# Optimization experiments

Measured on AMD Instinct MI355X. Metric: run time of the kernel, lower is better.

Reference implementation:

```python
import jax, jax.numpy as jnp
import numpy as np

PATCH = 14
LEVELS = 6
DIM = 512
MULT = 4
ITERS = 12
TOKEN_ATTEND_SELF_VALUE = -0.0005


def _grouped_ff(x, w1, b1, w2, b2):
    # x: [b, n, g, d]; per-group 1x1 conv == per-level MLP
    h = jnp.einsum('bnld,lmd->bnlm', x, w1) + b1  # [b,n,g,d*mult]
    h = jax.nn.gelu(h, approximate=False)
    return jnp.einsum('bnlm,ldm->bnld', h, w2) + b2


def _consensus(levels):
    # levels: [b, n, l, d]
    d = levels.shape[-1]
    n = levels.shape[1]
    k = levels / jnp.maximum(jnp.linalg.norm(levels, axis=-1, keepdims=True), 1e-12)
    sim = jnp.einsum('bild,bjld->blij', levels, k) * (d ** -0.5)
    self_mask = jnp.eye(n, dtype=bool)[None, None]  # attend_self=False
    sim = jnp.where(self_mask, TOKEN_ATTEND_SELF_VALUE, sim)
    attn = jax.nn.softmax(sim, axis=-1)
    return jnp.einsum('blij,bjld->bild', attn, levels)


def setup_inputs() -> dict:
    key = jax.random.key(0)
    ks = jax.random.split(key, 12)
    b, c, hw = 16, 1, 224
    pd = PATCH * PATCH * c  # 196
    nps = hw // PATCH
    n = nps * nps  # 256
    s = 0.02
    return {
        'img': jax.random.normal(ks[0], (b, c, hw, hw), jnp.float32),
        'to_tokens_w': jax.random.normal(ks[1], (pd, DIM), jnp.float32) * s,
        'to_tokens_b': jnp.zeros((DIM,), jnp.float32),
        'pos_emb': jax.random.normal(ks[2], (n, DIM), jnp.float32) * s,
        'init_levels': jax.random.normal(ks[3], (LEVELS, DIM), jnp.float32),
        'bu_w1': jax.random.normal(ks[4], (LEVELS, DIM * MULT, DIM), jnp.float32) * s,
        'bu_b1': jnp.zeros((LEVELS, DIM * MULT), jnp.float32),
        'bu_w2': jax.random.normal(ks[5], (LEVELS, DIM, DIM * MULT), jnp.float32) * s,
        'bu_b2': jnp.zeros((LEVELS, DIM), jnp.float32),
        'td_w1': jax.random.normal(ks[6], (LEVELS - 1, DIM * MULT, DIM), jnp.float32) * s,
        'td_b1': jnp.zeros((LEVELS - 1, DIM * MULT), jnp.float32),
        'td_w2': jax.random.normal(ks[7], (LEVELS - 1, DIM, DIM * MULT), jnp.float32) * s,
        'td_b2': jnp.zeros((LEVELS - 1, DIM), jnp.float32),
    }


def reference(img, to_tokens_w, to_tokens_b, pos_emb, init_levels,
              bu_w1, bu_b1, bu_w2, bu_b2, td_w1, td_b1, td_w2, td_b2):
    b, c, H, W = img.shape
    hp, wp = H // PATCH, W // PATCH
    n = hp * wp
    # b c (hp p1) (wp p2) -> b (hp wp) (p1 p2 c)
    x = img.reshape(b, c, hp, PATCH, wp, PATCH)
    x = x.transpose(0, 2, 4, 3, 5, 1).reshape(b, n, PATCH * PATCH * c)
    tokens = x @ to_tokens_w + to_tokens_b          # [b, n, d]
    pos = pos_emb[None, :, None, :]                 # [1, n, 1, d]
    bottom = tokens[:, :, None, :]                  # [b, n, 1, d]
    levels0 = jnp.broadcast_to(init_levels[None, None], (b, n, LEVELS, DIM))
    contrib = jnp.array([4., 4., 4., 4., 4., 3.], jnp.float32)[None, None, :, None]

    def step(levels, _):
        lwi = jnp.concatenate((bottom, levels), axis=2)         # [b, n, L+1, d]
        bu = _grouped_ff(lwi[:, :, :-1], bu_w1, bu_b1, bu_w2, bu_b2)
        td = _grouped_ff(lwi[:, :, 2:] + pos, td_w1, td_b1, td_w2, td_b2)
        td = jnp.pad(td, ((0, 0), (0, 0), (0, 1), (0, 0)))      # zero pad top level
        cons = _consensus(levels)
        new_levels = (levels + bu + td + cons) / contrib
        return new_levels, None

    levels, _ = jax.lax.scan(step, levels0, None, length=ITERS)
    return levels
```

## Files before the change

kernel.cpp:

```cpp
#include <hip/hip_runtime.h>
#include <hip/hip_bf16.h>
#include <math.h>

typedef unsigned short ushort_t;

#define DEV __device__ __forceinline__

DEV float bf2f(ushort_t u) {
  return __uint_as_float(((unsigned int)u) << 16);
}
DEV ushort_t f2bf(float f) {
  unsigned int x = __float_as_uint(f);
  return (ushort_t)((x + 0x7FFFu + ((x >> 16) & 1u)) >> 16);
}

DEV float gelu_f(float x) {
  float z = fabsf(x) * 0.70710678118654752f;
  float t = __builtin_amdgcn_rcpf(1.0f + 0.3275911f * z);
  float p = t * (0.254829592f +
            t * (-0.284496736f +
            t * (1.421413741f +
            t * (-1.453152027f +
            t * 1.061405429f))));
  float e = 1.0f - p * __expf(-z * z);
  float s = (x >= 0.f) ? e : -e;
  return 0.5f * x * (1.0f + s);
}

using bf16x8 = __attribute__((ext_vector_type(8))) __bf16;
using f32x4  = __attribute__((ext_vector_type(4))) float;

DEV void gload16(const ushort_t* g, ushort_t* l) {
  __builtin_amdgcn_global_load_lds((const __attribute__((address_space(1))) void*)g,
                                   (__attribute__((address_space(3))) void*)l, 16, 0, 0);
}

#define MFMA_QUAD(QM, QN)                                                      \
  _Pragma("unroll") for (int m_ = 0; m_ < 4; ++m_)                             \
  _Pragma("unroll") for (int n_ = 0; n_ < 2; ++n_)                             \
  _Pragma("unroll") for (int kk_ = 0; kk_ < 2; ++kk_)                          \
    acc[QM][QN][m_][n_] = __builtin_amdgcn_mfma_f32_16x16x32_bf16(             \
        aF[m_][kk_], bF[QN][n_][kk_], acc[QM][QN][m_][n_], 0, 0, 0);

template <typename F>
DEV void gemm256(const ushort_t* A, int lda, const ushort_t* B, int ldb, int K, F&& epi) {
  __shared__ alignas(16) ushort_t As[2][256 * 64];
  __shared__ alignas(16) ushort_t Bs[2][256 * 64];
  const int tid = threadIdx.x;
  const int lane = tid & 63;
  const int w = tid >> 6;
  const int ur = w >> 2, uc = w & 3;
  const int nk = K >> 6;

  const int c0 = tid, c1 = 512 + tid;
  const int row0 = c0 >> 3, row1 = c1 >> 3;
  const int sw0 = ((c0 & 7) ^ (row0 & 7)) * 8;
  const int sw1 = ((c1 & 7) ^ (row1 & 7)) * 8;
  const ushort_t* Ab0 = A + (size_t)row0 * lda + sw0;
  const ushort_t* Ab1 = A + (size_t)row1 * lda + sw1;
  const ushort_t* Bb0 = B + (size_t)row0 * ldb + sw0;
  const ushort_t* Bb1 = B + (size_t)row1 * ldb + sw1;
  const int ld0 = (0 * 512 + w * 64) * 8;
  const int ld1 = (1 * 512 + w * 64) * 8;

  auto stageA = [&](int t, int hh, int b) {
    const ushort_t* g0 = Ab0 + (size_t)hh * 128 * lda + t * 64;
    const ushort_t* g1 = Ab1 + (size_t)hh * 128 * lda + t * 64;
    ushort_t* l = &As[b][hh * 8192];
    gload16(g0, l + ld0);
    gload16(g1, l + ld1);
  };
  auto stageB = [&](int t, int hh, int b) {
    const ushort_t* g0 = Bb0 + (size_t)hh * 128 * ldb + t * 64;
    const ushort_t* g1 = Bb1 + (size_t)hh * 128 * ldb + t * 64;
    ushort_t* l = &Bs[b][hh * 8192];
    gload16(g0, l + ld0);
    gload16(g1, l + ld1);
  };

  int aoff[4][2], boff[2][2];
#pragma unroll
  for (int m = 0; m < 4; ++m)
#pragma unroll
    for (int kk = 0; kk < 2; ++kk) {
      int row = ur * 64 + m * 16 + (lane & 15);
      int ks = kk * 4 + (lane >> 4);
      aoff[m][kk] = row * 64 + ((ks ^ (lane & 7)) * 8);
    }
#pragma unroll
  for (int n = 0; n < 2; ++n)
#pragma unroll
    for (int kk = 0; kk < 2; ++kk) {
      int row = uc * 32 + n * 16 + (lane & 15);
      int ks = kk * 4 + (lane >> 4);
      boff[n][kk] = row * 64 + ((ks ^ (lane & 7)) * 8);
    }

  f32x4 acc[2][2][4][2];
#pragma unroll
  for (int qm = 0; qm < 2; ++qm)
#pragma unroll
    for (int qn = 0; qn < 2; ++qn)
#pragma unroll
      for (int m = 0; m < 4; ++m)
#pragma unroll
        for (int n = 0; n < 2; ++n) acc[qm][qn][m][n] = (f32x4){0.f, 0.f, 0.f, 0.f};

  stageA(0, 0, 0);
  stageB(0, 0, 0);
  stageB(0, 1, 0);
  stageA(0, 1, 0);
  stageA(1, 0, 1);
  stageB(1, 0, 1);
  asm volatile("s_waitcnt vmcnt(8)" ::: "memory");
  __builtin_amdgcn_s_barrier();

  bf16x8 aF[4][2], bF[2][2][2];

  for (int t = 0; t < nk; ++t) {
    const int b = t & 1;
    const ushort_t* asb = &As[b][0];
    const ushort_t* bsb = &Bs[b][0];
    const int t1 = (t + 1 < nk) ? t + 1 : nk - 1;
    const int t2 = (t + 2 < nk) ? t + 2 : nk - 1;

#pragma unroll
    for (int m = 0; m < 4; ++m)
#pragma unroll
      for (int kk = 0; kk < 2; ++kk) aF[m][kk] = *(const bf16x8*)&asb[aoff[m][kk]];
#pragma unroll
    for (int n = 0; n < 2; ++n)
#pragma unroll
      for (int kk = 0; kk < 2; ++kk) bF[0][n][kk] = *(const bf16x8*)&bsb[boff[n][kk]];
    stageB(t1, 1, (t + 1) & 1);
    __builtin_amdgcn_s_barrier();
    asm volatile("s_waitcnt lgkmcnt(0)" ::: "memory");
    __builtin_amdgcn_s_setprio(1);
    MFMA_QUAD(0, 0)
    __builtin_amdgcn_s_setprio(0);
    asm volatile("s_waitcnt vmcnt(8)" ::: "memory");
    __builtin_amdgcn_s_barrier();

#pragma unroll
    for (int n = 0; n < 2; ++n)
#pragma unroll
      for (int kk = 0; kk < 2; ++kk) bF[1][n][kk] = *(const bf16x8*)&bsb[boff[n][kk] + 8192];
    stageA(t1, 1, (t + 1) & 1);
    __builtin_amdgcn_s_barrier();
    asm volatile("s_waitcnt lgkmcnt(0)" ::: "memory");
    __builtin_amdgcn_s_setprio(1);
    MFMA_QUAD(0, 1)
    __builtin_amdgcn_s_setprio(0);
    asm volatile("s_waitcnt vmcnt(8)" ::: "memory");
    __builtin_amdgcn_s_barrier();

#pragma unroll
    for (int m = 0; m < 4; ++m)
#pragma unroll
      for (int kk = 0; kk < 2; ++kk) aF[m][kk] = *(const bf16x8*)&asb[aoff[m][kk] + 8192];
    stageA(t2, 0, b);
    __builtin_amdgcn_s_barrier();
    asm volatile("s_waitcnt lgkmcnt(0)" ::: "memory");
    __builtin_amdgcn_s_setprio(1);
    MFMA_QUAD(1, 0)
    __builtin_amdgcn_s_setprio(0);
    __builtin_amdgcn_s_barrier();

    stageB(t2, 0, b);
    __builtin_amdgcn_s_barrier();
    __builtin_amdgcn_s_setprio(1);
    MFMA_QUAD(1, 1)
    __builtin_amdgcn_s_setprio(0);
    asm volatile("s_waitcnt vmcnt(8)" ::: "memory");
    __builtin_amdgcn_s_barrier();
  }
  asm volatile("s_waitcnt vmcnt(0)" ::: "memory");

#pragma unroll
  for (int qm = 0; qm < 2; ++qm)
#pragma unroll
    for (int qn = 0; qn < 2; ++qn)
#pragma unroll
      for (int m = 0; m < 4; ++m)
#pragma unroll
        for (int n = 0; n < 2; ++n)
#pragma unroll
          for (int r = 0; r < 4; ++r) {
            int lr = qm * 128 + ur * 64 + m * 16 + (lane >> 4) * 4 + r;
            int lc = qn * 128 + uc * 32 + n * 16 + (lane & 15);
            epi(lr, lc, acc[qm][qn][m][n][r]);
          }
}

DEV void stage_tile(const ushort_t* g, int ld, ushort_t* lds, int t) {
  int w = t >> 6;
#pragma unroll
  for (int r = 0; r < 4; ++r) {
    int chunk = r * 256 + t;
    const ushort_t* gp = g + (size_t)(chunk >> 3) * ld + (size_t)(chunk & 7) * 8;
    ushort_t* lp = lds + (size_t)(r * 256 + w * 64) * 8;
    gload16(gp, lp);
  }
}

template <typename F>
DEV void gemm_tile(const ushort_t* A, int lda, const ushort_t* B, int ldb, int K, F&& epi) {
  __shared__ alignas(16) ushort_t As[128 * 64];
  __shared__ alignas(16) ushort_t Bs[128 * 64];
  int t = threadIdx.x;
  int lane = t & 63;
  int w = t >> 6;
  int wr = w >> 1, wc = w & 1;
  f32x4 zero = {0.f, 0.f, 0.f, 0.f};
  f32x4 acc[4][4];
#pragma unroll
  for (int m = 0; m < 4; ++m)
#pragma unroll
    for (int n = 0; n < 4; ++n) acc[m][n] = zero;

  for (int kt = 0; kt < K; kt += 64) {
    __syncthreads();
    stage_tile(A + kt, lda, As, t);
    stage_tile(B + kt, ldb, Bs, t);
    __syncthreads();
#pragma unroll
    for (int kk = 0; kk < 2; ++kk) {
      int kb = kk * 32 + (lane >> 4) * 8;
      bf16x8 af[4], bfr[4];
#pragma unroll
      for (int m = 0; m < 4; ++m)
        af[m] = *(const bf16x8*)&As[(size_t)(wr * 64 + m * 16 + (lane & 15)) * 64 + kb];
#pragma unroll
      for (int n = 0; n < 4; ++n)
        bfr[n] = *(const bf16x8*)&Bs[(size_t)(wc * 64 + n * 16 + (lane & 15)) * 64 + kb];
#pragma unroll
      for (int m = 0; m < 4; ++m)
#pragma unroll
        for (int n = 0; n < 4; ++n)
          acc[m][n] = __builtin_amdgcn_mfma_f32_16x16x32_bf16(af[m], bfr[n], acc[m][n], 0, 0, 0);
    }
  }
#pragma unroll
  for (int m = 0; m < 4; ++m)
#pragma unroll
    for (int n = 0; n < 4; ++n)
#pragma unroll
      for (int r = 0; r < 4; ++r) {
        int lr = wr * 64 + m * 16 + (lane >> 4) * 4 + r;
        int lc = wc * 64 + n * 16 + (lane & 15);
        epi(lr, lc, acc[m][n][r]);
      }
}

__global__ __launch_bounds__(256) void ff1_kernel(
    int g0, const ushort_t* tokens, const ushort_t* levels_bf, const ushort_t* levels_pos,
    const ushort_t* w1_bf, const float* bu_b1, const float* td_b1, ushort_t* h) {
  int g = g0 + blockIdx.z;
  int tm = blockIdx.x, tn = blockIdx.y;
  const ushort_t* A; int lda;
  if (g == 0)      { A = tokens     + (size_t)tm * 128 * 512;                              lda = 512;  }
  else if (g < 6)  { A = levels_bf  + (size_t)tm * 128 * 3072 + (size_t)(g - 1) * 512;     lda = 3072; }
  else             { A = levels_pos + (size_t)tm * 128 * 2560 + (size_t)(g - 6) * 512;     lda = 2560; }
  const ushort_t* W = w1_bf + (size_t)g * 2048 * 512 + (size_t)tn * 128 * 512;
  const float* bias = (g < 6) ? (bu_b1 + (size_t)g * 2048) : (td_b1 + (size_t)(g - 6) * 2048);
  ushort_t* out = h + ((size_t)(g - g0) * 4096 + (size_t)tm * 128) * 2048 + (size_t)tn * 128;
  gemm_tile(A, lda, W, 512, 512, [&](int lr, int lc, float v) {
    float x = v + bias[tn * 128 + lc];
    out[(size_t)lr * 2048 + lc] = f2bf(gelu_f(x));
  });
}

__global__ __launch_bounds__(512, 2) void ff2_kernel(
    int g0, const ushort_t* h, const ushort_t* w2_bf, const float* bu_b2, const float* td_b2,
    float* levels) {
  int g = g0 + blockIdx.z;
  int tm = blockIdx.x, tn = blockIdx.y;
  const ushort_t* A = h + ((size_t)(g - g0) * 4096 + (size_t)tm * 256) * 2048;
  const ushort_t* W = w2_bf + (size_t)g * 512 * 2048 + (size_t)tn * 256 * 2048;
  int l = (g < 6) ? g : (g - 6);
  const float* bias = (g < 6) ? (bu_b2 + (size_t)g * 512) : (td_b2 + (size_t)(g - 6) * 512);
  gemm256(A, 2048, W, 2048, 2048, [&](int lr, int lc, float v) {
    int bn = tm * 256 + lr;
    int d  = tn * 256 + lc;
    size_t idx = ((size_t)bn * 6 + l) * 512 + d;
    levels[idx] += v + bias[d];
  });
}

__global__ __launch_bounds__(256) void sim_kernel(const ushort_t* levels_bf, const float* invn,
                                                  ushort_t* simattn) {
  int bl = blockIdx.z; int tm = blockIdx.x, tn = blockIdx.y;
  int b = bl / 6, l = bl % 6;
  const ushort_t* A = levels_bf + ((size_t)(b * 256 + tm * 128) * 6 + l) * 512;
  const ushort_t* B = levels_bf + ((size_t)(b * 256 + tn * 128) * 6 + l) * 512;
  const float* inv = invn + (size_t)bl * 256;
  ushort_t* out = simattn + ((size_t)bl * 256 + tm * 128) * 256 + (size_t)tn * 128;
  gemm_tile(A, 3072, B, 3072, 512, [&](int lr, int lc, float v) {
    int i = tm * 128 + lr, j = tn * 128 + lc;
    float s = (i == j) ? -0.0005f : v * inv[j] * 0.044194173824159216f;
    out[(size_t)lr * 256 + lc] = f2bf(s);
  });
}

__global__ __launch_bounds__(256) void pv_kernel(const ushort_t* attn, const ushort_t* levelsT,
                                                 float* levels) {
  int bl = blockIdx.z; int tm = blockIdx.x, tn = blockIdx.y;
  int b = bl / 6, l = bl % 6;
  const ushort_t* A = attn + (size_t)bl * 256 * 256 + (size_t)tm * 128 * 256;
  const ushort_t* B = levelsT + ((size_t)bl * 512 + (size_t)tn * 128) * 256;
  gemm_tile(A, 256, B, 256, 256, [&](int lr, int lc, float v) {
    int n = tm * 128 + lr;
    int d = tn * 128 + lc;
    size_t idx = (((size_t)b * 256 + n) * 6 + l) * 512 + d;
    levels[idx] += v;
  });
}

__global__ __launch_bounds__(256) void softmax_kernel(ushort_t* simattn) {
  int row = blockIdx.x, t = threadIdx.x;
  __shared__ float red[256];
  float x = bf2f(simattn[(size_t)row * 256 + t]);
  red[t] = x;
  __syncthreads();
  for (int s = 128; s > 0; s >>= 1) { if (t < s) red[t] = fmaxf(red[t], red[t + s]); __syncthreads(); }
  float mx = red[0];
  __syncthreads();
  float e = expf(x - mx);
  red[t] = e;
  __syncthreads();
  for (int s = 128; s > 0; s >>= 1) { if (t < s) red[t] += red[t + s]; __syncthreads(); }
  float den = red[0];
  simattn[(size_t)row * 256 + t] = f2bf(e / den);
}

__global__ __launch_bounds__(128) void prep_kernel(float* levels, const float* pos_emb,
                                                   ushort_t* levels_bf, ushort_t* levels_pos,
                                                   float* invn, int apply) {
  int bid = blockIdx.x;
  int l = bid % 6;
  int bn = bid / 6;
  int n = bn & 255, b = bn >> 8;
  int t = threadIdx.x;
  float4 lv = *(const float4*)&levels[(size_t)bid * 512 + t * 4];
  if (apply) {
    float rc = (l == 5) ? (1.0f / 3.0f) : 0.25f;
    lv.x *= rc; lv.y *= rc; lv.z *= rc; lv.w *= rc;
    *(float4*)&levels[(size_t)bid * 512 + t * 4] = lv;
  }
  float ss = lv.x * lv.x + lv.y * lv.y + lv.z * lv.z + lv.w * lv.w;
#pragma unroll
  for (int off = 32; off > 0; off >>= 1) ss += __shfl_down(ss, off);
  __shared__ float s2[2];
  if ((t & 63) == 0) s2[t >> 6] = ss;
  __syncthreads();
  if (t == 0) {
    float tot = s2[0] + s2[1];
    invn[(size_t)(b * 6 + l) * 256 + n] = 1.0f / fmaxf(sqrtf(tot), 1e-12f);
  }
  ushort4 o;
  o.x = f2bf(lv.x); o.y = f2bf(lv.y); o.z = f2bf(lv.z); o.w = f2bf(lv.w);
  *(ushort4*)&levels_bf[(size_t)bid * 512 + t * 4] = o;
  if (l >= 1) {
    float4 pu = *(const float4*)&pos_emb[(size_t)n * 512 + t * 4];
    ushort4 op;
    op.x = f2bf(lv.x + pu.x);
    op.y = f2bf(lv.y + pu.y);
    op.z = f2bf(lv.z + pu.z);
    op.w = f2bf(lv.w + pu.w);
    *(ushort4*)&levels_pos[((size_t)bn * 5 + (l - 1)) * 512 + t * 4] = op;
  }
}

__global__ __launch_bounds__(256) void transpose_kernel(const float* levels, ushort_t* levelsT) {
  int bl = blockIdx.z; int b = bl / 6, l = bl % 6;
  int n0 = blockIdx.y * 64, d0 = blockIdx.x * 64;
  __shared__ ushort_t tile[64][72];
  int t = threadIdx.x;
#pragma unroll
  for (int rr = 0; rr < 2; ++rr) {
    int c = t + rr * 256;
    int r = c >> 3, c8 = (c & 7) * 8;
    const float* src = &levels[(((size_t)(b * 256 + n0 + r)) * 6 + l) * 512 + d0 + c8];
    float4 v0 = *(const float4*)src;
    float4 v1 = *(const float4*)(src + 4);
    tile[r][c8 + 0] = f2bf(v0.x); tile[r][c8 + 1] = f2bf(v0.y);
    tile[r][c8 + 2] = f2bf(v0.z); tile[r][c8 + 3] = f2bf(v0.w);
    tile[r][c8 + 4] = f2bf(v1.x); tile[r][c8 + 5] = f2bf(v1.y);
    tile[r][c8 + 6] = f2bf(v1.z); tile[r][c8 + 7] = f2bf(v1.w);
  }
  __syncthreads();
#pragma unroll
  for (int rr = 0; rr < 2; ++rr) {
    int c = t + rr * 256;
    int dr = c >> 3, n8 = (c & 7) * 8;
    ushort4 o0, o1;
    o0.x = tile[n8 + 0][dr]; o0.y = tile[n8 + 1][dr]; o0.z = tile[n8 + 2][dr]; o0.w = tile[n8 + 3][dr];
    o1.x = tile[n8 + 4][dr]; o1.y = tile[n8 + 5][dr]; o1.z = tile[n8 + 6][dr]; o1.w = tile[n8 + 7][dr];
    ushort_t* dst = &levelsT[((size_t)bl * 512 + d0 + dr) * 256 + n0 + n8];
    *(ushort4*)dst = o0;
    *(ushort4*)(dst + 4) = o1;
  }
}

__global__ __launch_bounds__(256) void tokens_kernel(const float* img, const float* ttw,
                                                     const float* ttb, ushort_t* tokens) {
  int token = blockIdx.x;
  int b = token >> 8, n = token & 255;
  int ph = n >> 4, pw = n & 15;
  __shared__ float patch[196];
  int t = threadIdx.x;
  if (t < 196) {
    int r = t / 14, cc = t % 14;
    patch[t] = img[(size_t)b * 50176 + (size_t)(ph * 14 + r) * 224 + pw * 14 + cc];
  }
  __syncthreads();
  float a0 = ttb[t];
  float a1 = ttb[t + 256];
  for (int k = 0; k < 196; ++k) {
    float p = patch[k];
    a0 += p * ttw[(size_t)k * 512 + t];
    a1 += p * ttw[(size_t)k * 512 + t + 256];
  }
  tokens[(size_t)token * 512 + t]       = f2bf(a0);
  tokens[(size_t)token * 512 + t + 256] = f2bf(a1);
}

__global__ void init_kernel(const float* init_levels, float* levels) {
  size_t i4 = (size_t)blockIdx.x * 256 + threadIdx.x;
  size_t e0 = i4 * 4;
  int idx = (int)(e0 % 3072);
  *(float4*)&levels[e0] = *(const float4*)&init_levels[idx];
}

__global__ void scale_kernel(float* levels) {
  size_t i4 = (size_t)blockIdx.x * 256 + threadIdx.x;
  size_t e0 = i4 * 4;
  int l = (int)((e0 >> 9) % 6);
  float rc = (l == 5) ? (1.0f / 3.0f) : 0.25f;
  float4 a = *(const float4*)&levels[e0];
  float4 o = {a.x * rc, a.y * rc, a.z * rc, a.w * rc};
  *(float4*)&levels[e0] = o;
}

__global__ void cvt_kernel(const float* src, ushort_t* dst, int n4) {
  int i = blockIdx.x * 256 + threadIdx.x;
  if (i >= n4) return;
  float4 v = ((const float4*)src)[i];
  ushort4 o;
  o.x = f2bf(v.x); o.y = f2bf(v.y); o.z = f2bf(v.z); o.w = f2bf(v.w);
  ((ushort4*)dst)[i] = o;
}

extern "C" void kernel_launch(void* const* d_in, const int* in_sizes, int n_in,
                              void* d_out, int out_size, void* d_ws, size_t ws_size,
                              hipStream_t stream) {
  const float* img    = (const float*)d_in[0];
  const float* ttw    = (const float*)d_in[1];
  const float* ttb    = (const float*)d_in[2];
  const float* pos    = (const float*)d_in[3];
  const float* initlv = (const float*)d_in[4];
  const float* bu_w1  = (const float*)d_in[5];
  const float* bu_b1  = (const float*)d_in[6];
  const float* bu_w2  = (const float*)d_in[7];
  const float* bu_b2  = (const float*)d_in[8];
  const float* td_w1  = (const float*)d_in[9];
  const float* td_b1  = (const float*)d_in[10];
  const float* td_w2  = (const float*)d_in[11];
  const float* td_b2  = (const float*)d_in[12];

  float* levels = (float*)d_out;

  char* p = (char*)d_ws;
  auto alloc = [&](size_t bytes) { char* r = p; p += (bytes + 255) & ~(size_t)255; return r; };
  float*    invn       = (float*)alloc(24576ull * 4);
  ushort_t* tokens     = (ushort_t*)alloc(2097152ull * 2);
  ushort_t* levels_bf  = (ushort_t*)alloc(12582912ull * 2);
  ushort_t* levels_pos = (ushort_t*)alloc(10485760ull * 2);
  ushort_t* levelsT    = (ushort_t*)alloc(12582912ull * 2);
  ushort_t* simattn    = (ushort_t*)alloc(6291456ull * 2);
  ushort_t* w1_bf      = (ushort_t*)alloc(11534336ull * 2);
  ushort_t* w2_bf      = (ushort_t*)alloc(11534336ull * 2);
  size_t used = (size_t)(p - (char*)d_ws);
  if (used + 16777216ull > ws_size) return;
  size_t hbytes = ws_size - used;
  int gpp = (int)(hbytes / 16777216ull);
  if (gpp > 6) gpp = 6;
  ushort_t* h = (ushort_t*)alloc((size_t)gpp * 16777216ull);

  cvt_kernel<<<6144, 256, 0, stream>>>(bu_w1, w1_bf, 1572864);
  cvt_kernel<<<5120, 256, 0, stream>>>(td_w1, w1_bf + 6291456ull, 1310720);
  cvt_kernel<<<6144, 256, 0, stream>>>(bu_w2, w2_bf, 1572864);
  cvt_kernel<<<5120, 256, 0, stream>>>(td_w2, w2_bf + 6291456ull, 1310720);
  tokens_kernel<<<4096, 256, 0, stream>>>(img, ttw, ttb, tokens);
  init_kernel<<<12288, 256, 0, stream>>>(initlv, levels);

  for (int it = 0; it < 12; ++it) {
    prep_kernel<<<24576, 128, 0, stream>>>(levels, pos, levels_bf, levels_pos, invn,
                                           it > 0 ? 1 : 0);
    transpose_kernel<<<dim3(8, 4, 96), 256, 0, stream>>>(levels, levelsT);
    sim_kernel<<<dim3(2, 2, 96), 256, 0, stream>>>(levels_bf, invn, simattn);
    softmax_kernel<<<24576, 256, 0, stream>>>(simattn);
    pv_kernel<<<dim3(2, 4, 96), 256, 0, stream>>>(simattn, levelsT, levels);
    for (int g0 = 0; g0 < 11; g0 += gpp) {
      int gn = 11 - g0 < gpp ? 11 - g0 : gpp;
      ff1_kernel<<<dim3(32, 16, gn), 256, 0, stream>>>(g0, tokens, levels_bf, levels_pos,
                                                       w1_bf, bu_b1, td_b1, h);
      ff2_kernel<<<dim3(16, 2, gn), 512, 0, stream>>>(g0, h, w2_bf, bu_b2, td_b2, levels);
    }
  }
  scale_kernel<<<12288, 256, 0, stream>>>(levels);
}
```

Measured before the change: 5.540 ms.

## Fuse similarity and softmax, enlarge FF1 tiles, batch all FF groups

Replaces the separate sim GEMM and row-softmax kernels with one kernel that computes a full 128x256 similarity tile per block and does the row max/sum reduction in registers and shared memory. This removes a round trip of the bf16 score matrix through global memory and one launch per iteration. FF1 moves to a 256x256 tile GEMM with 512 threads but drops double buffering, so loads are no longer overlapped with compute. When the workspace is large enough, all 11 groups are launched at once rather than in chunks of six, giving fewer and larger launches. The fused kernel exposes fewer blocks, which may lower occupancy.

```diff
diff --git a/kernel.cpp b/kernel.cpp
--- a/kernel.cpp
+++ b/kernel.cpp
@@ -33,6 +33,76 @@
 DEV void gload16(const ushort_t* g, ushort_t* l) {
   __builtin_amdgcn_global_load_lds((const __attribute__((address_space(1))) void*)g,
                                    (__attribute__((address_space(3))) void*)l, 16, 0, 0);
+}
+
+DEV void stage256(const ushort_t* g, int ld, ushort_t* lds, int t) {
+  int w = t >> 6;
+#pragma unroll
+  for (int r = 0; r < 4; ++r) {
+    int chunk = r * 512 + t;
+    const ushort_t* gp = g + (size_t)(chunk >> 3) * ld + (size_t)(chunk & 7) * 8;
+    ushort_t* lp = lds + (size_t)(r * 512 + w * 64) * 8;
+    gload16(gp, lp);
+  }
+}
+
+DEV void stage128_512(const ushort_t* g, int ld, ushort_t* lds, int t) {
+  int w = t >> 6;
+#pragma unroll
+  for (int r = 0; r < 2; ++r) {
+    int chunk = r * 512 + t;
+    const ushort_t* gp = g + (size_t)(chunk >> 3) * ld + (size_t)(chunk & 7) * 8;
+    ushort_t* lp = lds + (size_t)(r * 512 + w * 64) * 8;
+    gload16(gp, lp);
+  }
+}
+
+template <typename F>
+DEV void gemm256_2ph(const ushort_t* A, int lda, const ushort_t* B, int ldb, int K, F&& epi) {
+  __shared__ alignas(16) ushort_t As[256 * 64];
+  __shared__ alignas(16) ushort_t Bs[256 * 64];
+  int t = threadIdx.x;
+  int lane = t & 63;
+  int w = t >> 6;
+  int ur = w >> 2, uc = w & 3;
+  f32x4 acc[8][4];
+#pragma unroll
+  for (int m = 0; m < 8; ++m)
+#pragma unroll
+    for (int n = 0; n < 4; ++n) acc[m][n] = (f32x4){0.f, 0.f, 0.f, 0.f};
+
+  for (int kt = 0; kt < K; kt += 64) {
+    __syncthreads();
+    stage256(A + kt, lda, As, t);
+    stage256(B + kt, ldb, Bs, t);
+    __syncthreads();
+#pragma unroll
+    for (int kk = 0; kk < 2; ++kk) {
+      int kb = kk * 32 + (lane >> 4) * 8;
+      bf16x8 af[8], bfr[4];
+#pragma unroll
+      for (int m = 0; m < 8; ++m)
+        af[m] = *(const bf16x8*)&As[(size_t)(ur * 128 + m * 16 + (lane & 15)) * 64 + kb];
+#pragma unroll
+      for (int n = 0; n < 4; ++n)
+        bfr[n] = *(const bf16x8*)&Bs[(size_t)(uc * 64 + n * 16 + (lane & 15)) * 64 + kb];
+#pragma unroll
+      for (int m = 0; m < 8; ++m)
+#pragma unroll
+        for (int n = 0; n < 4; ++n)
+          acc[m][n] = __builtin_amdgcn_mfma_f32_16x16x32_bf16(af[m], bfr[n], acc[m][n], 0, 0, 0);
+    }
+  }
+#pragma unroll
+  for (int m = 0; m < 8; ++m)
+#pragma unroll
+    for (int n = 0; n < 4; ++n)
+#pragma unroll
+      for (int r = 0; r < 4; ++r) {
+        int lr = ur * 128 + m * 16 + (lane >> 4) * 4 + r;
+        int lc = uc * 64 + n * 16 + (lane & 15);
+        epi(lr, lc, acc[m][n][r]);
+      }
 }
 
 #define MFMA_QUAD(QM, QN)                                                      \
@@ -252,20 +322,20 @@
       }
 }
 
-__global__ __launch_bounds__(256) void ff1_kernel(
+__global__ __launch_bounds__(512, 2) void ff1_kernel(
     int g0, const ushort_t* tokens, const ushort_t* levels_bf, const ushort_t* levels_pos,
     const ushort_t* w1_bf, const float* bu_b1, const float* td_b1, ushort_t* h) {
   int g = g0 + blockIdx.z;
   int tm = blockIdx.x, tn = blockIdx.y;
   const ushort_t* A; int lda;
-  if (g == 0)      { A = tokens     + (size_t)tm * 128 * 512;                              lda = 512;  }
-  else if (g < 6)  { A = levels_bf  + (size_t)tm * 128 * 3072 + (size_t)(g - 1) * 512;     lda = 3072; }
-  else             { A = levels_pos + (size_t)tm * 128 * 2560 + (size_t)(g - 6) * 512;     lda = 2560; }
-  const ushort_t* W = w1_bf + (size_t)g * 2048 * 512 + (size_t)tn * 128 * 512;
+  if (g == 0)      { A = tokens     + (size_t)tm * 256 * 512;                              lda = 512;  }
+  else if (g < 6)  { A = levels_bf  + (size_t)tm * 256 * 3072 + (size_t)(g - 1) * 512;     lda = 3072; }
+  else             { A = levels_pos + (size_t)tm * 256 * 2560 + (size_t)(g - 6) * 512;     lda = 2560; }
+  const ushort_t* W = w1_bf + (size_t)g * 2048 * 512 + (size_t)tn * 256 * 512;
   const float* bias = (g < 6) ? (bu_b1 + (size_t)g * 2048) : (td_b1 + (size_t)(g - 6) * 2048);
-  ushort_t* out = h + ((size_t)(g - g0) * 4096 + (size_t)tm * 128) * 2048 + (size_t)tn * 128;
-  gemm_tile(A, lda, W, 512, 512, [&](int lr, int lc, float v) {
-    float x = v + bias[tn * 128 + lc];
+  ushort_t* out = h + ((size_t)(g - g0) * 4096 + (size_t)tm * 256) * 2048 + (size_t)tn * 256;
+  gemm256_2ph(A, lda, W, 512, 512, [&](int lr, int lc, float v) {
+    float x = v + bias[tn * 256 + lc];
     out[(size_t)lr * 2048 + lc] = f2bf(gelu_f(x));
   });
 }
@@ -287,19 +357,143 @@
   });
 }
 
-__global__ __launch_bounds__(256) void sim_kernel(const ushort_t* levels_bf, const float* invn,
-                                                  ushort_t* simattn) {
-  int bl = blockIdx.z; int tm = blockIdx.x, tn = blockIdx.y;
+__global__ __launch_bounds__(512) void simsm_kernel(const ushort_t* levels_bf, const float* invn,
+                                                    ushort_t* attn) {
+  int tm = blockIdx.x;
+  int bl = blockIdx.y;
   int b = bl / 6, l = bl % 6;
   const ushort_t* A = levels_bf + ((size_t)(b * 256 + tm * 128) * 6 + l) * 512;
-  const ushort_t* B = levels_bf + ((size_t)(b * 256 + tn * 128) * 6 + l) * 512;
+  const ushort_t* B = levels_bf + ((size_t)(b * 256) * 6 + l) * 512;
   const float* inv = invn + (size_t)bl * 256;
-  ushort_t* out = simattn + ((size_t)bl * 256 + tm * 128) * 256 + (size_t)tn * 128;
-  gemm_tile(A, 3072, B, 3072, 512, [&](int lr, int lc, float v) {
-    int i = tm * 128 + lr, j = tn * 128 + lc;
-    float s = (i == j) ? -0.0005f : v * inv[j] * 0.044194173824159216f;
-    out[(size_t)lr * 256 + lc] = f2bf(s);
-  });
+  ushort_t* out = attn + ((size_t)(bl * 256 + tm * 128)) * 256;
+
+  __shared__ alignas(16) ushort_t As[128 * 64];
+  __shared__ alignas(16) ushort_t Bs[256 * 64];
+  __shared__ alignas(16) float red[128][4];
+
+  int t = threadIdx.x, lane = t & 63, w = t >> 6;
+  int ur = w >> 2, uc = w & 3;
+  f32x4 acc[4][4];
+#pragma unroll
+  for (int m = 0; m < 4; ++m)
+#pragma unroll
+    for (int n = 0; n < 4; ++n) acc[m][n] = (f32x4){0.f, 0.f, 0.f, 0.f};
+
+  for (int kt = 0; kt < 512; kt += 64) {
+    __syncthreads();
+    stage128_512(A + kt, 3072, As, t);
+    stage256(B + kt, 3072, Bs, t);
+    __syncthreads();
+#pragma unroll
+    for (int kk = 0; kk < 2; ++kk) {
+      int kb = kk * 32 + (lane >> 4) * 8;
+      bf16x8 af[4], bfr[4];
+#pragma unroll
+      for (int m = 0; m < 4; ++m)
+        af[m] = *(const bf16x8*)&As[(size_t)(ur * 64 + m * 16 + (lane & 15)) * 64 + kb];
+#pragma unroll
+      for (int n = 0; n < 4; ++n)
+        bfr[n] = *(const bf16x8*)&Bs[(size_t)(uc * 64 + n * 16 + (lane & 15)) * 64 + kb];
+#pragma unroll
+      for (int m = 0; m < 4; ++m)
+#pragma unroll
+        for (int n = 0; n < 4; ++n)
+          acc[m][n] = __builtin_amdgcn_mfma_f32_16x16x32_bf16(af[m], bfr[n], acc[m][n], 0, 0, 0);
+    }
+  }
+
+  float invv[4];
+#pragma unroll
+  for (int n = 0; n < 4; ++n)
+    invv[n] = inv[uc * 64 + n * 16 + (lane & 15)] * 0.044194173824159216f;
+  float rowm[4][4];
+#pragma unroll
+  for (int m = 0; m < 4; ++m)
+#pragma unroll
+    for (int r = 0; r < 4; ++r) rowm[m][r] = -3.0e38f;
+#pragma unroll
+  for (int m = 0; m < 4; ++m)
+#pragma unroll
+    for (int n = 0; n < 4; ++n)
+#pragma unroll
+      for (int r = 0; r < 4; ++r) {
+        int i = tm * 128 + ur * 64 + m * 16 + (lane >> 4) * 4 + r;
+        int j = uc * 64 + n * 16 + (lane & 15);
+        float v = (i == j) ? -0.0005f : acc[m][n][r] * invv[n];
+        acc[m][n][r] = v;
+        rowm[m][r] = fmaxf(rowm[m][r], v);
+      }
+#pragma unroll
+  for (int off = 1; off < 16; off <<= 1)
+#pragma unroll
+    for (int m = 0; m < 4; ++m)
+#pragma unroll
+      for (int r = 0; r < 4; ++r) rowm[m][r] = fmaxf(rowm[m][r], __shfl_xor(rowm[m][r], off));
+  if ((lane & 15) == 0) {
+#pragma unroll
+    for (int m = 0; m < 4; ++m)
+#pragma unroll
+      for (int r = 0; r < 4; ++r)
+        red[ur * 64 + m * 16 + (lane >> 4) * 4 + r][uc] = rowm[m][r];
+  }
+  __syncthreads();
+  float rmax[4][4];
+#pragma unroll
+  for (int m = 0; m < 4; ++m)
+#pragma unroll
+    for (int r = 0; r < 4; ++r) {
+      float4 p = *(const float4*)&red[ur * 64 + m * 16 + (lane >> 4) * 4 + r][0];
+      rmax[m][r] = fmaxf(fmaxf(p.x, p.y), fmaxf(p.z, p.w));
+    }
+  __syncthreads();
+
+  float rows[4][4];
+#pragma unroll
+  for (int m = 0; m < 4; ++m)
+#pragma unroll
+    for (int r = 0; r < 4; ++r) rows[m][r] = 0.f;
+#pragma unroll
+  for (int m = 0; m < 4; ++m)
+#pragma unroll
+    for (int n = 0; n < 4; ++n)
+#pragma unroll
+      for (int r = 0; r < 4; ++r) {
+        float e = __expf(acc[m][n][r] - rmax[m][r]);
+        acc[m][n][r] = e;
+        rows[m][r] += e;
+      }
+#pragma unroll
+  for (int off = 1; off < 16; off <<= 1)
+#pragma unroll
+    for (int m = 0; m < 4; ++m)
+#pragma unroll
+      for (int r = 0; r < 4; ++r) rows[m][r] += __shfl_xor(rows[m][r], off);
+  if ((lane & 15) == 0) {
+#pragma unroll
+    for (int m = 0; m < 4; ++m)
+#pragma unroll
+      for (int r = 0; r < 4; ++r)
+        red[ur * 64 + m * 16 + (lane >> 4) * 4 + r][uc] = rows[m][r];
+  }
+  __syncthreads();
+  float rden[4][4];
+#pragma unroll
+  for (int m = 0; m < 4; ++m)
+#pragma unroll
+    for (int r = 0; r < 4; ++r) {
+      float4 p = *(const float4*)&red[ur * 64 + m * 16 + (lane >> 4) * 4 + r][0];
+      rden[m][r] = __builtin_amdgcn_rcpf(p.x + p.y + p.z + p.w);
+    }
+#pragma unroll
+  for (int m = 0; m < 4; ++m)
+#pragma unroll
+    for (int n = 0; n < 4; ++n)
+#pragma unroll
+      for (int r = 0; r < 4; ++r) {
+        int lr = ur * 64 + m * 16 + (lane >> 4) * 4 + r;
+        int lc = uc * 64 + n * 16 + (lane & 15);
+        out[(size_t)lr * 256 + lc] = f2bf(acc[m][n][r] * rden[m][r]);
+      }
 }
 
 __global__ __launch_bounds__(256) void pv_kernel(const ushort_t* attn, const ushort_t* levelsT,
@@ -314,23 +508,6 @@
     size_t idx = (((size_t)b * 256 + n) * 6 + l) * 512 + d;
     levels[idx] += v;
   });
-}
-
-__global__ __launch_bounds__(256) void softmax_kernel(ushort_t* simattn) {
-  int row = blockIdx.x, t = threadIdx.x;
-  __shared__ float red[256];
-  float x = bf2f(simattn[(size_t)row * 256 + t]);
-  red[t] = x;
-  __syncthreads();
-  for (int s = 128; s > 0; s >>= 1) { if (t < s) red[t] = fmaxf(red[t], red[t + s]); __syncthreads(); }
-  float mx = red[0];
-  __syncthreads();
-  float e = expf(x - mx);
-  red[t] = e;
-  __syncthreads();
-  for (int s = 128; s > 0; s >>= 1) { if (t < s) red[t] += red[t + s]; __syncthreads(); }
-  float den = red[0];
-  simattn[(size_t)row * 256 + t] = f2bf(e / den);
 }
 
 __global__ __launch_bounds__(128) void prep_kernel(float* levels, const float* pos_emb,
@@ -483,9 +660,9 @@
   size_t used = (size_t)(p - (char*)d_ws);
   if (used + 16777216ull > ws_size) return;
   size_t hbytes = ws_size - used;
-  int gpp = (int)(hbytes / 16777216ull);
-  if (gpp > 6) gpp = 6;
-  ushort_t* h = (ushort_t*)alloc((size_t)gpp * 16777216ull);
+  int hgroups = (int)(hbytes / 16777216ull);
+  if (hgroups > 11) hgroups = 11;
+  ushort_t* h = (ushort_t*)alloc((size_t)hgroups * 16777216ull);
 
   cvt_kernel<<<6144, 256, 0, stream>>>(bu_w1, w1_bf, 1572864);
   cvt_kernel<<<5120, 256, 0, stream>>>(td_w1, w1_bf + 6291456ull, 1310720);
@@ -498,14 +675,22 @@
     prep_kernel<<<24576, 128, 0, stream>>>(levels, pos, levels_bf, levels_pos, invn,
                                            it > 0 ? 1 : 0);
     transpose_kernel<<<dim3(8, 4, 96), 256, 0, stream>>>(levels, levelsT);
-    sim_kernel<<<dim3(2, 2, 96), 256, 0, stream>>>(levels_bf, invn, simattn);
-    softmax_kernel<<<24576, 256, 0, stream>>>(simattn);
+    simsm_kernel<<<dim3(2, 96), 512, 0, stream>>>(levels_bf, invn, simattn);
     pv_kernel<<<dim3(2, 4, 96), 256, 0, stream>>>(simattn, levelsT, levels);
-    for (int g0 = 0; g0 < 11; g0 += gpp) {
-      int gn = 11 - g0 < gpp ? 11 - g0 : gpp;
-      ff1_kernel<<<dim3(32, 16, gn), 256, 0, stream>>>(g0, tokens, levels_bf, levels_pos,
-                                                       w1_bf, bu_b1, td_b1, h);
-      ff2_kernel<<<dim3(16, 2, gn), 512, 0, stream>>>(g0, h, w2_bf, bu_b2, td_b2, levels);
+    if (hgroups >= 11) {
+      ff1_kernel<<<dim3(16, 8, 11), 512, 0, stream>>>(0, tokens, levels_bf, levels_pos,
+                                                      w1_bf, bu_b1, td_b1, h);
+      ff2_kernel<<<dim3(16, 2, 6), 512, 0, stream>>>(0, h, w2_bf, bu_b2, td_b2, levels);
+      ff2_kernel<<<dim3(16, 2, 5), 512, 0, stream>>>(6, h + 50331648ull, w2_bf,
+                                                     bu_b2, td_b2, levels);
+    } else {
+      int gpp = hgroups < 6 ? hgroups : 6;
+      for (int g0 = 0; g0 < 11; g0 += gpp) {
+        int gn = 11 - g0 < gpp ? 11 - g0 : gpp;
+        ff1_kernel<<<dim3(16, 8, gn), 512, 0, stream>>>(g0, tokens, levels_bf, levels_pos,
+                                                        w1_bf, bu_b1, td_b1, h);
+        ff2_kernel<<<dim3(16, 2, gn), 512, 0, stream>>>(g0, h, w2_bf, bu_b2, td_b2, levels);
+      }
     }
   }
   scale_kernel<<<12288, 256, 0, stream>>>(levels);
```

Measured after the change: 5.969 ms. +7.8%, slower.

## Use 256x256 single-buffer GEMM tiles for FF1 and batch all FF groups per launch

Applied to the files above, without the earlier changes.

FF1 moves from 128x128 tiles with 256 threads to a new 256x256 tile GEMM with 512 threads, which stages both operands into LDS and computes 8x4 MFMA fragments per wave. This raises data reuse per tile at the cost of no double buffering. The top-down FF2 outputs are now written to a separate fp32 buffer and added in prep/scale, which removes the read-modify-write race across levels. With that in place, all 11 groups can run in one launch when workspace allows. Softmax also switches to the fast __expf.

```diff
diff --git a/kernel.cpp b/kernel.cpp
--- a/kernel.cpp
+++ b/kernel.cpp
@@ -33,6 +33,65 @@
 DEV void gload16(const ushort_t* g, ushort_t* l) {
   __builtin_amdgcn_global_load_lds((const __attribute__((address_space(1))) void*)g,
                                    (__attribute__((address_space(3))) void*)l, 16, 0, 0);
+}
+
+DEV void stage256(const ushort_t* g, int ld, ushort_t* lds, int t) {
+  int w = t >> 6;
+#pragma unroll
+  for (int r = 0; r < 4; ++r) {
+    int chunk = r * 512 + t;
+    const ushort_t* gp = g + (size_t)(chunk >> 3) * ld + (size_t)(chunk & 7) * 8;
+    ushort_t* lp = lds + (size_t)(r * 512 + w * 64) * 8;
+    gload16(gp, lp);
+  }
+}
+
+template <typename F>
+DEV void gemm256_2ph(const ushort_t* A, int lda, const ushort_t* B, int ldb, int K, F&& epi) {
+  __shared__ alignas(16) ushort_t As[256 * 64];
+  __shared__ alignas(16) ushort_t Bs[256 * 64];
+  int t = threadIdx.x;
+  int lane = t & 63;
+  int w = t >> 6;
+  int ur = w >> 2, uc = w & 3;
+  f32x4 acc[8][4];
+#pragma unroll
+  for (int m = 0; m < 8; ++m)
+#pragma unroll
+    for (int n = 0; n < 4; ++n) acc[m][n] = (f32x4){0.f, 0.f, 0.f, 0.f};
+
+  for (int kt = 0; kt < K; kt += 64) {
+    __syncthreads();
+    stage256(A + kt, lda, As, t);
+    stage256(B + kt, ldb, Bs, t);
+    __syncthreads();
+#pragma unroll
+    for (int kk = 0; kk < 2; ++kk) {
+      int kb = kk * 32 + (lane >> 4) * 8;
+      bf16x8 af[8], bfr[4];
+#pragma unroll
+      for (int m = 0; m < 8; ++m)
+        af[m] = *(const bf16x8*)&As[(size_t)(ur * 128 + m * 16 + (lane & 15)) * 64 + kb];
+#pragma unroll
+      for (int n = 0; n < 4; ++n)
+        bfr[n] = *(const bf16x8*)&Bs[(size_t)(uc * 64 + n * 16 + (lane & 15)) * 64 + kb];
+#pragma unroll
+      for (int m = 0; m < 8; ++m)
+#pragma unroll
+        for (int n = 0; n < 4; ++n)
+          acc[m][n] = __builtin_amdgcn_mfma_f32_16x16x32_bf16(af[m], bfr[n], acc[m][n], 0, 0, 0);
+    }
+  }
+#pragma unroll
+  for (int m = 0; m < 8; ++m)
+#pragma unroll
+    for (int n = 0; n < 4; ++n)
+#pragma unroll
+      for (int r = 0; r < 4; ++r) {
+        int lr = ur * 128 + m * 16 + (lane >> 4) * 4 + r;
+        int lc = uc * 64 + n * 16 + (lane & 15);
+        epi(lr, lc, acc[m][n][r]);
+      }
 }
 
 #define MFMA_QUAD(QM, QN)                                                      \
@@ -252,38 +311,40 @@
       }
 }
 
-__global__ __launch_bounds__(256) void ff1_kernel(
+__global__ __launch_bounds__(512, 2) void ff1_kernel(
     int g0, const ushort_t* tokens, const ushort_t* levels_bf, const ushort_t* levels_pos,
     const ushort_t* w1_bf, const float* bu_b1, const float* td_b1, ushort_t* h) {
   int g = g0 + blockIdx.z;
   int tm = blockIdx.x, tn = blockIdx.y;
   const ushort_t* A; int lda;
-  if (g == 0)      { A = tokens     + (size_t)tm * 128 * 512;                              lda = 512;  }
-  else if (g < 6)  { A = levels_bf  + (size_t)tm * 128 * 3072 + (size_t)(g - 1) * 512;     lda = 3072; }
-  else             { A = levels_pos + (size_t)tm * 128 * 2560 + (size_t)(g - 6) * 512;     lda = 2560; }
-  const ushort_t* W = w1_bf + (size_t)g * 2048 * 512 + (size_t)tn * 128 * 512;
+  if (g == 0)      { A = tokens     + (size_t)tm * 256 * 512;                              lda = 512;  }
+  else if (g < 6)  { A = levels_bf  + (size_t)tm * 256 * 3072 + (size_t)(g - 1) * 512;     lda = 3072; }
+  else             { A = levels_pos + (size_t)tm * 256 * 2560 + (size_t)(g - 6) * 512;     lda = 2560; }
+  const ushort_t* W = w1_bf + (size_t)g * 2048 * 512 + (size_t)tn * 256 * 512;
   const float* bias = (g < 6) ? (bu_b1 + (size_t)g * 2048) : (td_b1 + (size_t)(g - 6) * 2048);
-  ushort_t* out = h + ((size_t)(g - g0) * 4096 + (size_t)tm * 128) * 2048 + (size_t)tn * 128;
-  gemm_tile(A, lda, W, 512, 512, [&](int lr, int lc, float v) {
-    float x = v + bias[tn * 128 + lc];
+  ushort_t* out = h + ((size_t)(g - g0) * 4096 + (size_t)tm * 256) * 2048 + (size_t)tn * 256;
+  gemm256_2ph(A, lda, W, 512, 512, [&](int lr, int lc, float v) {
+    float x = v + bias[tn * 256 + lc];
     out[(size_t)lr * 2048 + lc] = f2bf(gelu_f(x));
   });
 }
 
 __global__ __launch_bounds__(512, 2) void ff2_kernel(
     int g0, const ushort_t* h, const ushort_t* w2_bf, const float* bu_b2, const float* td_b2,
-    float* levels) {
+    float* levels, float* tdbuf) {
   int g = g0 + blockIdx.z;
   int tm = blockIdx.x, tn = blockIdx.y;
   const ushort_t* A = h + ((size_t)(g - g0) * 4096 + (size_t)tm * 256) * 2048;
   const ushort_t* W = w2_bf + (size_t)g * 512 * 2048 + (size_t)tn * 256 * 2048;
   int l = (g < 6) ? g : (g - 6);
   const float* bias = (g < 6) ? (bu_b2 + (size_t)g * 512) : (td_b2 + (size_t)(g - 6) * 512);
+  bool to_td = (g >= 6) && (tdbuf != nullptr);
   gemm256(A, 2048, W, 2048, 2048, [&](int lr, int lc, float v) {
     int bn = tm * 256 + lr;
     int d  = tn * 256 + lc;
-    size_t idx = ((size_t)bn * 6 + l) * 512 + d;
-    levels[idx] += v + bias[d];
+    float r = v + bias[d];
+    if (to_td) tdbuf[((size_t)bn * 5 + l) * 512 + d] = r;
+    else       levels[((size_t)bn * 6 + l) * 512 + d] += r;
   });
 }
 
@@ -302,6 +363,23 @@
   });
 }
 
+__global__ __launch_bounds__(256) void softmax_kernel(ushort_t* simattn) {
+  int row = blockIdx.x, t = threadIdx.x;
+  __shared__ float red[256];
+  float x = bf2f(simattn[(size_t)row * 256 + t]);
+  red[t] = x;
+  __syncthreads();
+  for (int s = 128; s > 0; s >>= 1) { if (t < s) red[t] = fmaxf(red[t], red[t + s]); __syncthreads(); }
+  float mx = red[0];
+  __syncthreads();
+  float e = __expf(x - mx);
+  red[t] = e;
+  __syncthreads();
+  for (int s = 128; s > 0; s >>= 1) { if (t < s) red[t] += red[t + s]; __syncthreads(); }
+  float den = red[0];
+  simattn[(size_t)row * 256 + t] = f2bf(e / den);
+}
+
 __global__ __launch_bounds__(256) void pv_kernel(const ushort_t* attn, const ushort_t* levelsT,
                                                  float* levels) {
   int bl = blockIdx.z; int tm = blockIdx.x, tn = blockIdx.y;
@@ -316,26 +394,9 @@
   });
 }
 
-__global__ __launch_bounds__(256) void softmax_kernel(ushort_t* simattn) {
-  int row = blockIdx.x, t = threadIdx.x;
-  __shared__ float red[256];
-  float x = bf2f(simattn[(size_t)row * 256 + t]);
-  red[t] = x;
-  __syncthreads();
-  for (int s = 128; s > 0; s >>= 1) { if (t < s) red[t] = fmaxf(red[t], red[t + s]); __syncthreads(); }
-  float mx = red[0];
-  __syncthreads();
-  float e = expf(x - mx);
-  red[t] = e;
-  __syncthreads();
-  for (int s = 128; s > 0; s >>= 1) { if (t < s) red[t] += red[t + s]; __syncthreads(); }
-  float den = red[0];
-  simattn[(size_t)row * 256 + t] = f2bf(e / den);
-}
-
 __global__ __launch_bounds__(128) void prep_kernel(float* levels, const float* pos_emb,
                                                    ushort_t* levels_bf, ushort_t* levels_pos,
-                                                   float* invn, int apply) {
+                                                   float* invn, const float* tdbuf, int apply) {
   int bid = blockIdx.x;
   int l = bid % 6;
   int bn = bid / 6;
@@ -343,6 +404,10 @@
   int t = threadIdx.x;
   float4 lv = *(const float4*)&levels[(size_t)bid * 512 + t * 4];
   if (apply) {
+    if (tdbuf != nullptr && l < 5) {
+      float4 td = *(const float4*)&tdbuf[((size_t)bn * 5 + l) * 512 + t * 4];
+      lv.x += td.x; lv.y += td.y; lv.z += td.z; lv.w += td.w;
+    }
     float rc = (l == 5) ? (1.0f / 3.0f) : 0.25f;
     lv.x *= rc; lv.y *= rc; lv.z *= rc; lv.w *= rc;
     *(float4*)&levels[(size_t)bid * 512 + t * 4] = lv;
@@ -432,12 +497,18 @@
   *(float4*)&levels[e0] = *(const float4*)&init_levels[idx];
 }
 
-__global__ void scale_kernel(float* levels) {
+__global__ void scale_kernel(float* levels, const float* tdbuf) {
   size_t i4 = (size_t)blockIdx.x * 256 + threadIdx.x;
   size_t e0 = i4 * 4;
   int l = (int)((e0 >> 9) % 6);
+  size_t bn = e0 / 3072;
+  int d = (int)(e0 & 511);
+  float4 a = *(const float4*)&levels[e0];
+  if (tdbuf != nullptr && l < 5) {
+    float4 td = *(const float4*)&tdbuf[((size_t)bn * 5 + l) * 512 + d];
+    a.x += td.x; a.y += td.y; a.z += td.z; a.w += td.w;
+  }
   float rc = (l == 5) ? (1.0f / 3.0f) : 0.25f;
-  float4 a = *(const float4*)&levels[e0];
   float4 o = {a.x * rc, a.y * rc, a.z * rc, a.w * rc};
   *(float4*)&levels[e0] = o;
 }
@@ -470,6 +541,9 @@
 
   float* levels = (float*)d_out;
 
+  const size_t HB = 16777216ull;
+  const size_t TDB = 10485760ull * 4;
+
   char* p = (char*)d_ws;
   auto alloc = [&](size_t bytes) { char* r = p; p += (bytes + 255) & ~(size_t)255; return r; };
   float*    invn       = (float*)alloc(24576ull * 4);
@@ -481,11 +555,15 @@
   ushort_t* w1_bf      = (ushort_t*)alloc(11534336ull * 2);
   ushort_t* w2_bf      = (ushort_t*)alloc(11534336ull * 2);
   size_t used = (size_t)(p - (char*)d_ws);
-  if (used + 16777216ull > ws_size) return;
-  size_t hbytes = ws_size - used;
-  int gpp = (int)(hbytes / 16777216ull);
-  if (gpp > 6) gpp = 6;
-  ushort_t* h = (ushort_t*)alloc((size_t)gpp * 16777216ull);
+
+  float* tdbuf = nullptr;
+  if (used + TDB + HB + 512 <= ws_size) tdbuf = (float*)alloc(TDB);
+  used = (size_t)(p - (char*)d_ws);
+  if (used + HB > ws_size) return;
+  int hgroups = (int)((ws_size - used) / HB);
+  int hcap = tdbuf ? 11 : 6;
+  if (hgroups > hcap) hgroups = hcap;
+  ushort_t* h = (ushort_t*)alloc((size_t)hgroups * HB);
 
   cvt_kernel<<<6144, 256, 0, stream>>>(bu_w1, w1_bf, 1572864);
   cvt_kernel<<<5120, 256, 0, stream>>>(td_w1, w1_bf + 6291456ull, 1310720);
@@ -496,17 +574,18 @@
 
   for (int it = 0; it < 12; ++it) {
     prep_kernel<<<24576, 128, 0, stream>>>(levels, pos, levels_bf, levels_pos, invn,
-                                           it > 0 ? 1 : 0);
+                                           tdbuf, it > 0 ? 1 : 0);
     transpose_kernel<<<dim3(8, 4, 96), 256, 0, stream>>>(levels, levelsT);
     sim_kernel<<<dim3(2, 2, 96), 256, 0, stream>>>(levels_bf, invn, simattn);
     softmax_kernel<<<24576, 256, 0, stream>>>(simattn);
     pv_kernel<<<dim3(2, 4, 96), 256, 0, stream>>>(simattn, levelsT, levels);
-    for (int g0 = 0; g0 < 11; g0 += gpp) {
-      int gn = 11 - g0 < gpp ? 11 - g0 : gpp;
-      ff1_kernel<<<dim3(32, 16, gn), 256, 0, stream>>>(g0, tokens, levels_bf, levels_pos,
-                                                       w1_bf, bu_b1, td_b1, h);
-      ff2_kernel<<<dim3(16, 2, gn), 512, 0, stream>>>(g0, h, w2_bf, bu_b2, td_b2, levels);
+    for (int g0 = 0; g0 < 11; g0 += hgroups) {
+      int gn = 11 - g0 < hgroups ? 11 - g0 : hgroups;
+      ff1_kernel<<<dim3(16, 8, gn), 512, 0, stream>>>(g0, tokens, levels_bf, levels_pos,
+                                                      w1_bf, bu_b1, td_b1, h);
+      ff2_kernel<<<dim3(16, 2, gn), 512, 0, stream>>>(g0, h, w2_bf, bu_b2, td_b2,
+                                                      levels, tdbuf);
     }
   }
-  scale_kernel<<<12288, 256, 0, stream>>>(levels);
-}
+  scale_kernel<<<12288, 256, 0, stream>>>(levels, tdbuf);
+}
```

Result: slower. 8.296 ms (+49.8%).

## Double-buffer 128x128 GEMM tile with XOR-swizzled LDS and faster softmax exp

Applied to the files above, without the earlier changes.

Rewrites the shared 128x128 gemm_tile used by ff1, sim and pv kernels so it double-buffers LDS tiles. The next K-slice is fetched with async global_load_lds while the current one feeds MFMA, and waits use vmcnt plus raw barriers instead of two __syncthreads per iteration. LDS columns are XOR-swizzled to reduce bank conflicts, and MFMA bursts run at raised wave priority. Softmax switches expf to __expf, trading a little accuracy for speed. The change doubles LDS use per block, which may lower occupancy.

```diff
diff --git a/kernel.cpp b/kernel.cpp
--- a/kernel.cpp
+++ b/kernel.cpp
@@ -33,6 +33,87 @@
 DEV void gload16(const ushort_t* g, ushort_t* l) {
   __builtin_amdgcn_global_load_lds((const __attribute__((address_space(1))) void*)g,
                                    (__attribute__((address_space(3))) void*)l, 16, 0, 0);
+}
+
+DEV void stage_sw(const ushort_t* g, int ld, ushort_t* lds, int t) {
+  int w = t >> 6;
+#pragma unroll
+  for (int r = 0; r < 4; ++r) {
+    int chunk = r * 256 + t;
+    int row = chunk >> 3;
+    int sw  = ((chunk & 7) ^ (row & 7)) * 8;
+    const ushort_t* gp = g + (size_t)row * ld + sw;
+    ushort_t* lp = lds + (size_t)(r * 256 + w * 64) * 8;
+    gload16(gp, lp);
+  }
+}
+
+template <typename F>
+DEV void gemm_tile(const ushort_t* A, int lda, const ushort_t* B, int ldb, int K, F&& epi) {
+  __shared__ alignas(16) ushort_t As[2][128 * 64];
+  __shared__ alignas(16) ushort_t Bs[2][128 * 64];
+  int t = threadIdx.x;
+  int lane = t & 63;
+  int w = t >> 6;
+  int wr = w >> 1, wc = w & 1;
+  const int nk = K >> 6;
+  f32x4 acc[4][4];
+#pragma unroll
+  for (int m = 0; m < 4; ++m)
+#pragma unroll
+    for (int n = 0; n < 4; ++n) acc[m][n] = (f32x4){0.f, 0.f, 0.f, 0.f};
+
+  int aoff[4][2], boff[4][2];
+#pragma unroll
+  for (int m = 0; m < 4; ++m)
+#pragma unroll
+    for (int kk = 0; kk < 2; ++kk) {
+      int ks = kk * 4 + (lane >> 4);
+      aoff[m][kk] = (wr * 64 + m * 16 + (lane & 15)) * 64 + ((ks ^ (lane & 7)) * 8);
+      boff[m][kk] = (wc * 64 + m * 16 + (lane & 15)) * 64 + ((ks ^ (lane & 7)) * 8);
+    }
+
+  stage_sw(A, lda, As[0], t);
+  stage_sw(B, ldb, Bs[0], t);
+
+  for (int kt = 0; kt < nk; ++kt) {
+    int cur = kt & 1;
+    int nxt = (kt + 1 < nk) ? kt + 1 : kt;
+    stage_sw(A + (size_t)nxt * 64, lda, As[cur ^ 1], t);
+    stage_sw(B + (size_t)nxt * 64, ldb, Bs[cur ^ 1], t);
+    asm volatile("s_waitcnt vmcnt(8)" ::: "memory");
+    __builtin_amdgcn_s_barrier();
+    __builtin_amdgcn_sched_barrier(0);
+    const ushort_t* asb = &As[cur][0];
+    const ushort_t* bsb = &Bs[cur][0];
+#pragma unroll
+    for (int kk = 0; kk < 2; ++kk) {
+      bf16x8 af[4], bfr[4];
+#pragma unroll
+      for (int m = 0; m < 4; ++m) af[m] = *(const bf16x8*)&asb[aoff[m][kk]];
+#pragma unroll
+      for (int n = 0; n < 4; ++n) bfr[n] = *(const bf16x8*)&bsb[boff[n][kk]];
+      __builtin_amdgcn_s_setprio(1);
+#pragma unroll
+      for (int m = 0; m < 4; ++m)
+#pragma unroll
+        for (int n = 0; n < 4; ++n)
+          acc[m][n] = __builtin_amdgcn_mfma_f32_16x16x32_bf16(af[m], bfr[n], acc[m][n], 0, 0, 0);
+      __builtin_amdgcn_s_setprio(0);
+    }
+    __builtin_amdgcn_s_barrier();
+  }
+
+#pragma unroll
+  for (int m = 0; m < 4; ++m)
+#pragma unroll
+    for (int n = 0; n < 4; ++n)
+#pragma unroll
+      for (int r = 0; r < 4; ++r) {
+        int lr = wr * 64 + m * 16 + (lane >> 4) * 4 + r;
+        int lc = wc * 64 + n * 16 + (lane & 15);
+        epi(lr, lc, acc[m][n][r]);
+      }
 }
 
 #define MFMA_QUAD(QM, QN)                                                      \
@@ -190,66 +271,6 @@
             int lc = qn * 128 + uc * 32 + n * 16 + (lane & 15);
             epi(lr, lc, acc[qm][qn][m][n][r]);
           }
-}
-
-DEV void stage_tile(const ushort_t* g, int ld, ushort_t* lds, int t) {
-  int w = t >> 6;
-#pragma unroll
-  for (int r = 0; r < 4; ++r) {
-    int chunk = r * 256 + t;
-    const ushort_t* gp = g + (size_t)(chunk >> 3) * ld + (size_t)(chunk & 7) * 8;
-    ushort_t* lp = lds + (size_t)(r * 256 + w * 64) * 8;
-    gload16(gp, lp);
-  }
-}
-
-template <typename F>
-DEV void gemm_tile(const ushort_t* A, int lda, const ushort_t* B, int ldb, int K, F&& epi) {
-  __shared__ alignas(16) ushort_t As[128 * 64];
-  __shared__ alignas(16) ushort_t Bs[128 * 64];
-  int t = threadIdx.x;
-  int lane = t & 63;
-  int w = t >> 6;
-  int wr = w >> 1, wc = w & 1;
-  f32x4 zero = {0.f, 0.f, 0.f, 0.f};
-  f32x4 acc[4][4];
-#pragma unroll
-  for (int m = 0; m < 4; ++m)
-#pragma unroll
-    for (int n = 0; n < 4; ++n) acc[m][n] = zero;
-
-  for (int kt = 0; kt < K; kt += 64) {
-    __syncthreads();
-    stage_tile(A + kt, lda, As, t);
-    stage_tile(B + kt, ldb, Bs, t);
-    __syncthreads();
-#pragma unroll
-    for (int kk = 0; kk < 2; ++kk) {
-      int kb = kk * 32 + (lane >> 4) * 8;
-      bf16x8 af[4], bfr[4];
-#pragma unroll
-      for (int m = 0; m < 4; ++m)
-        af[m] = *(const bf16x8*)&As[(size_t)(wr * 64 + m * 16 + (lane & 15)) * 64 + kb];
-#pragma unroll
-      for (int n = 0; n < 4; ++n)
-        bfr[n] = *(const bf16x8*)&Bs[(size_t)(wc * 64 + n * 16 + (lane & 15)) * 64 + kb];
-#pragma unroll
-      for (int m = 0; m < 4; ++m)
-#pragma unroll
-        for (int n = 0; n < 4; ++n)
-          acc[m][n] = __builtin_amdgcn_mfma_f32_16x16x32_bf16(af[m], bfr[n], acc[m][n], 0, 0, 0);
-    }
-  }
-#pragma unroll
-  for (int m = 0; m < 4; ++m)
-#pragma unroll
-    for (int n = 0; n < 4; ++n)
-#pragma unroll
-      for (int r = 0; r < 4; ++r) {
-        int lr = wr * 64 + m * 16 + (lane >> 4) * 4 + r;
-        int lc = wc * 64 + n * 16 + (lane & 15);
-        epi(lr, lc, acc[m][n][r]);
-      }
 }
 
 __global__ __launch_bounds__(256) void ff1_kernel(
@@ -302,6 +323,23 @@
   });
 }
 
+__global__ __launch_bounds__(256) void softmax_kernel(ushort_t* simattn) {
+  int row = blockIdx.x, t = threadIdx.x;
+  __shared__ float red[256];
+  float x = bf2f(simattn[(size_t)row * 256 + t]);
+  red[t] = x;
+  __syncthreads();
+  for (int s = 128; s > 0; s >>= 1) { if (t < s) red[t] = fmaxf(red[t], red[t + s]); __syncthreads(); }
+  float mx = red[0];
+  __syncthreads();
+  float e = __expf(x - mx);
+  red[t] = e;
+  __syncthreads();
+  for (int s = 128; s > 0; s >>= 1) { if (t < s) red[t] += red[t + s]; __syncthreads(); }
+  float den = red[0];
+  simattn[(size_t)row * 256 + t] = f2bf(e / den);
+}
+
 __global__ __launch_bounds__(256) void pv_kernel(const ushort_t* attn, const ushort_t* levelsT,
                                                  float* levels) {
   int bl = blockIdx.z; int tm = blockIdx.x, tn = blockIdx.y;
@@ -314,23 +352,6 @@
     size_t idx = (((size_t)b * 256 + n) * 6 + l) * 512 + d;
     levels[idx] += v;
   });
-}
-
-__global__ __launch_bounds__(256) void softmax_kernel(ushort_t* simattn) {
-  int row = blockIdx.x, t = threadIdx.x;
-  __shared__ float red[256];
-  float x = bf2f(simattn[(size_t)row * 256 + t]);
-  red[t] = x;
-  __syncthreads();
-  for (int s = 128; s > 0; s >>= 1) { if (t < s) red[t] = fmaxf(red[t], red[t + s]); __syncthreads(); }
-  float mx = red[0];
-  __syncthreads();
-  float e = expf(x - mx);
-  red[t] = e;
-  __syncthreads();
-  for (int s = 128; s > 0; s >>= 1) { if (t < s) red[t] += red[t + s]; __syncthreads(); }
-  float den = red[0];
-  simattn[(size_t)row * 256 + t] = f2bf(e / den);
 }
 
 __global__ __launch_bounds__(128) void prep_kernel(float* levels, const float* pos_emb,
@@ -470,6 +491,8 @@
 
   float* levels = (float*)d_out;
 
+  const size_t HB = 16777216ull;
+
   char* p = (char*)d_ws;
   auto alloc = [&](size_t bytes) { char* r = p; p += (bytes + 255) & ~(size_t)255; return r; };
   float*    invn       = (float*)alloc(24576ull * 4);
@@ -481,11 +504,10 @@
   ushort_t* w1_bf      = (ushort_t*)alloc(11534336ull * 2);
   ushort_t* w2_bf      = (ushort_t*)alloc(11534336ull * 2);
   size_t used = (size_t)(p - (char*)d_ws);
-  if (used + 16777216ull > ws_size) return;
-  size_t hbytes = ws_size - used;
-  int gpp = (int)(hbytes / 16777216ull);
+  if (used + HB > ws_size) return;
+  int gpp = (int)((ws_size - used) / HB);
   if (gpp > 6) gpp = 6;
-  ushort_t* h = (ushort_t*)alloc((size_t)gpp * 16777216ull);
+  ushort_t* h = (ushort_t*)alloc((size_t)gpp * HB);
 
   cvt_kernel<<<6144, 256, 0, stream>>>(bu_w1, w1_bf, 1572864);
   cvt_kernel<<<5120, 256, 0, stream>>>(td_w1, w1_bf + 6291456ull, 1310720);
```

After: 5.595 ms. About the same (+1.0%).
